# Kernel optimization log

Hardware: AMD Instinct MI355X
Metric: run time of the kernel (lower is better)

Reference implementation:

```python
import jax, jax.numpy as jnp
import numpy as np

N = 100000   # nodes
E = 1600000  # edges
IN = 128     # in_node_channels
H = 128      # hidden_channels
EPS = 1e-5   # BatchNorm eps


def _gcn_conv(x, W, b, src, dst, n):
    # x' = W x, then symmetric-normalized aggregation with self-loops (PyG GCNConv)
    xw = x @ W                                             # [N, H]
    loop = jnp.arange(n, dtype=src.dtype)
    src_f = jnp.concatenate([src, loop])                   # [E+N]
    dst_f = jnp.concatenate([dst, loop])
    deg = jax.ops.segment_sum(jnp.ones(src_f.shape, xw.dtype), dst_f, num_segments=n)
    dis = jax.lax.rsqrt(jnp.maximum(deg, 1.0))             # deg >= 1 due to self-loops
    norm = dis[src_f] * dis[dst_f]                         # [E+N]
    msg = xw[src_f] * norm[:, None]                        # gather + scale
    out = jax.ops.segment_sum(msg, dst_f, num_segments=n)  # scatter-add
    return out + b


def _bn(x, gamma, beta):
    # training-mode BatchNorm1d over the node dimension
    m = jnp.mean(x, axis=0)
    v = jnp.mean(jnp.square(x - m), axis=0)
    return gamma * (x - m) * jax.lax.rsqrt(v + EPS) + beta


def setup_inputs() -> dict:
    key = jax.random.key(0)
    ks = jax.random.split(key, 8)
    glorot = lambda k, shape, fan: jax.random.normal(k, shape, jnp.float32) / np.sqrt(fan).astype(np.float32)
    x = jax.random.normal(ks[0], (N, IN), jnp.float32)
    edge_index = jax.random.randint(ks[1], (2, E), 0, N, dtype=jnp.int32)
    return {
        "x": x,
        "edge_index": edge_index,
        "W1": glorot(ks[2], (IN, H), IN), "b1": jnp.zeros((H,), jnp.float32),
        "g1": jnp.ones((H,), jnp.float32), "be1": jnp.zeros((H,), jnp.float32),
        "W2": glorot(ks[3], (H, H), H), "b2": jnp.zeros((H,), jnp.float32),
        "g2": jnp.ones((H,), jnp.float32), "be2": jnp.zeros((H,), jnp.float32),
        "Wm1": glorot(ks[4], (H, 64), H), "bm1": jnp.zeros((64,), jnp.float32),
        "Wm2": glorot(ks[5], (64, 1), 64), "bm2": jnp.zeros((1,), jnp.float32),
    }


def reference(x, edge_index, W1, b1, g1, be1, W2, b2, g2, be2, Wm1, bm1, Wm2, bm2):
    src, dst = edge_index[0], edge_index[1]
    h = jax.nn.relu(_bn(_gcn_conv(x, W1, b1, src, dst, N), g1, be1))
    h = jax.nn.relu(_bn(_gcn_conv(h, W2, b2, src, dst, N), g2, be2))
    # MLP head (dropout is identity in eval / deterministic reference)
    h = jax.nn.relu(h @ Wm1 + bm1)
    out = h @ Wm2 + bm2                                     # [N, 1]
    return jnp.squeeze(out, axis=-1)                        # [N]
```

## Files before the change

kernel.cpp:

```cpp
#include <hip/hip_runtime.h>
#include <hip/hip_fp16.h>

#define HC 128
#define EPS_BN 1e-5f
#define NSTRIPE 8
#define AGG_BLOCKS 3072
#define BSHIFT 9
#define BNODES (1 << BSHIFT)
#define BCAP 12288
#define CHUNK 8192
#define SRC_BITS 18

typedef _Float16 f16;
typedef f16  f16x8 __attribute__((ext_vector_type(8)));
typedef float f32x4 __attribute__((ext_vector_type(4)));

__global__ void prologue(const float* __restrict__ W1, const float* __restrict__ W2,
                         const float* __restrict__ Wm1,
                         f16* __restrict__ Wt1, f16* __restrict__ Wt2,
                         f16* __restrict__ Wm1t, f16* __restrict__ padrow,
                         int* __restrict__ gcur, float* __restrict__ stats) {
    int idx = blockIdx.x * 256 + threadIdx.x;
    if (idx < 16384) {
        int k = idx >> 7, c = idx & 127;
        Wt1[(size_t)c * HC + k] = (f16)W1[idx];
    } else if (idx < 32768) {
        int i = idx - 16384;
        int k = i >> 7, c = i & 127;
        Wt2[(size_t)c * HC + k] = (f16)W2[i];
    } else if (idx < 40960) {
        int i = idx - 32768;
        int c = i >> 7, k = i & 127;
        Wm1t[(size_t)c * HC + k] = (f16)Wm1[(size_t)k * 64 + c];
    } else if (idx < 41088) {
        padrow[idx - 40960] = (f16)0.f;
    } else if (idx < 41344) {
        int b = idx - 41088;
        gcur[b] = b * BCAP;
    } else if (idx < 45440) {
        stats[idx - 41344] = 0.f;
    }
}

__global__ __launch_bounds__(1024) void edge_bin(const int* __restrict__ src,
                                                 const int* __restrict__ dst,
                                                 int* __restrict__ gcur,
                                                 unsigned int* __restrict__ packed, int E) {
    __shared__ int cnt[256];
    __shared__ int cur[256];
    const int tid = threadIdx.x;
    const int e0 = blockIdx.x * CHUNK;
    if (tid < 256) cnt[tid] = 0;
    __syncthreads();
    for (int i = tid; i < CHUNK; i += 1024) {
        int e = e0 + i;
        if (e < E) atomicAdd(&cnt[dst[e] >> BSHIFT], 1);
    }
    __syncthreads();
    if (tid < 256) cur[tid] = (cnt[tid] > 0) ? atomicAdd(&gcur[tid], cnt[tid]) : 0;
    __syncthreads();
    for (int i = tid; i < CHUNK; i += 1024) {
        int e = e0 + i;
        if (e < E) {
            int s = src[e], d = dst[e];
            int pos = atomicAdd(&cur[d >> BSHIFT], 1);
            packed[pos] = ((unsigned)(d & (BNODES - 1)) << SRC_BITS) | (unsigned)s;
        }
    }
}

__global__ __launch_bounds__(1024) void edge_sort(const unsigned int* __restrict__ packed,
                                                  const int* __restrict__ gcur,
                                                  int2* __restrict__ rowptr2,
                                                  float* __restrict__ dis,
                                                  int* __restrict__ srcs, int n) {
    __shared__ int cnt[BNODES];
    __shared__ int cur[BNODES];
    __shared__ int scn[BNODES];
    const int b = blockIdx.x;
    const int node0 = b << BSHIFT;
    const int tid = threadIdx.x;
    const int base = b * BCAP;
    const int end  = gcur[b];

    if (tid < BNODES) cnt[tid] = 0;
    __syncthreads();
    for (int e = base + tid; e < end; e += 1024)
        atomicAdd(&cnt[packed[e] >> SRC_BITS], 1);
    __syncthreads();
    if (tid < BNODES) scn[tid] = cnt[tid];
    __syncthreads();
    for (int off = 1; off < BNODES; off <<= 1) {
        int t = 0;
        if (tid < BNODES && tid >= off) t = scn[tid - off];
        __syncthreads();
        if (tid < BNODES) scn[tid] += t;
        __syncthreads();
    }
    if (tid < BNODES) {
        int excl = scn[tid] - cnt[tid];
        int node = node0 + tid;
        if (node < n) {
            rowptr2[node] = make_int2(base + excl, base + excl + cnt[tid]);
            dis[node] = rsqrtf((float)cnt[tid] + 1.f);
        }
        cur[tid] = excl;
    }
    __syncthreads();
    for (int e = base + tid; e < end; e += 1024) {
        unsigned p = packed[e];
        int pos = atomicAdd(&cur[p >> SRC_BITS], 1);
        srcs[base + pos] = (int)(p & ((1u << SRC_BITS) - 1));
    }
}

template<int SRC_F16, int TRANS>
__global__ __launch_bounds__(256) void gemm_mfma(const void* __restrict__ Xv,
                                                 const f16* __restrict__ Wt,
                                                 const float* __restrict__ stats,
                                                 const float* __restrict__ gamma,
                                                 const float* __restrict__ beta,
                                                 const float* __restrict__ dis,
                                                 f16* __restrict__ Y, int n) {
    __shared__ f16 Ah[64][136];
    __shared__ f16 Bh[128][136];
    __shared__ float sc[HC], sh[HC];
    const int tid  = threadIdx.x;
    const int row0 = blockIdx.x * 64;

    if constexpr (TRANS) {
        if (tid < 128) {
            float s = 0.f, q = 0.f;
#pragma unroll
            for (int t = 0; t < NSTRIPE; ++t) {
                s += stats[t * 256 + tid];
                q += stats[t * 256 + 128 + tid];
            }
            float m = s / (float)n;
            float v = q / (float)n - m * m;
            float scv = gamma[tid] * rsqrtf(fmaxf(v, 0.f) + EPS_BN);
            sc[tid] = scv;
            sh[tid] = beta[tid] - m * scv;
        }
    }

#pragma unroll
    for (int i = 0; i < 8; ++i) {
        int idx = i * 256 + tid;
        int r = idx >> 4, g = idx & 15;
        *(f16x8*)&Bh[r][g * 8] = *(const f16x8*)(Wt + (size_t)r * HC + g * 8);
    }
    __syncthreads();

#pragma unroll
    for (int i = 0; i < 4; ++i) {
        int idx = i * 256 + tid;
        int r = idx >> 4, g = idx & 15;
        int grow = row0 + r;
        f16x8 h = {};
        if (grow < n) {
            if constexpr (SRC_F16) {
                f16x8 v = *(const f16x8*)((const f16*)Xv + (size_t)grow * HC + g * 8);
                if constexpr (TRANS) {
#pragma unroll
                    for (int j = 0; j < 8; ++j) {
                        float f = (float)v[j];
                        f = fmaxf(fmaf(f, sc[g * 8 + j], sh[g * 8 + j]), 0.f);
                        h[j] = (f16)f;
                    }
                } else h = v;
            } else {
                const float* X = (const float*)Xv;
                float4 a = *(const float4*)(X + (size_t)grow * HC + g * 8);
                float4 c = *(const float4*)(X + (size_t)grow * HC + g * 8 + 4);
                h[0] = (f16)a.x; h[1] = (f16)a.y; h[2] = (f16)a.z; h[3] = (f16)a.w;
                h[4] = (f16)c.x; h[5] = (f16)c.y; h[6] = (f16)c.z; h[7] = (f16)c.w;
            }
        }
        *(f16x8*)&Ah[r][g * 8] = h;
    }
    __syncthreads();

    const int wv   = tid >> 6;
    const int lane = tid & 63;
    const int m    = lane & 15;
    const int kq   = (lane >> 4) * 8;

    f32x4 acc[8] = {};
#pragma unroll
    for (int kc = 0; kc < HC; kc += 32) {
        f16x8 a = *(const f16x8*)&Ah[wv * 16 + m][kc + kq];
#pragma unroll
        for (int t = 0; t < 8; ++t) {
            f16x8 b = *(const f16x8*)&Bh[t * 16 + m][kc + kq];
            acc[t] = __builtin_amdgcn_mfma_f32_16x16x32_f16(a, b, acc[t], 0, 0, 0);
        }
    }

    const int rbase = row0 + wv * 16 + (lane >> 4) * 4;
#pragma unroll
    for (int r = 0; r < 4; ++r) {
        int grow = rbase + r;
        if (grow < n) {
            float dv = dis[grow];
#pragma unroll
            for (int t = 0; t < 8; ++t)
                Y[(size_t)grow * HC + t * 16 + m] = (f16)(acc[t][r] * dv);
        }
    }
}

__global__ __launch_bounds__(256) void gcn_agg_f16(const f16* __restrict__ xws,
                                                   const int* __restrict__ srcs,
                                                   const int2* __restrict__ rowptr2,
                                                   const float* __restrict__ dis,
                                                   const float* __restrict__ bias,
                                                   f16* __restrict__ out,
                                                   float* __restrict__ stats,
                                                   int n, int nwaves) {
    __shared__ float lds_s[4][128], lds_q[4][128];
    const int wv   = threadIdx.x >> 6;
    const int lane = threadIdx.x & 63;
    const int g    = lane >> 4;
    const int cg   = lane & 15;

    float b8[8];
#pragma unroll
    for (int j = 0; j < 8; ++j) b8[j] = bias[cg * 8 + j];

    float s8[8] = {}, q8[8] = {};

    for (int node = blockIdx.x * 4 + wv; node < n; node += nwaves) {
        const int2 rp = rowptr2[node];
        const int e1 = rp.y;
        float acc[8] = {};
        for (int e = rp.x; e < e1; e += 8) {
            int i0 = e + g, i1 = e + g + 4;
            int s0 = (i0 < e1) ? srcs[i0] : n;
            int s1 = (i1 < e1) ? srcs[i1] : n;
            f16x8 v0 = *(const f16x8*)(xws + (size_t)s0 * HC + cg * 8);
            f16x8 v1 = *(const f16x8*)(xws + (size_t)s1 * HC + cg * 8);
#pragma unroll
            for (int j = 0; j < 8; ++j) {
                acc[j] += (float)v0[j];
                acc[j] += (float)v1[j];
            }
        }
#pragma unroll
        for (int j = 0; j < 8; ++j) acc[j] += __shfl_xor(acc[j], 16);
#pragma unroll
        for (int j = 0; j < 8; ++j) acc[j] += __shfl_xor(acc[j], 32);

        if (g == 0) {
            float dv = dis[node];
            f16x8 self = *(const f16x8*)(xws + (size_t)node * HC + cg * 8);
            f16x8 o;
#pragma unroll
            for (int j = 0; j < 8; ++j) {
                float r = fmaf(acc[j] + (float)self[j], dv, b8[j]);
                o[j] = (f16)r;
                s8[j] += r;
                q8[j] += r * r;
            }
            *(f16x8*)(out + (size_t)node * HC + cg * 8) = o;
        }
    }

    if (g == 0) {
#pragma unroll
        for (int j = 0; j < 8; ++j) {
            lds_s[wv][cg * 8 + j] = s8[j];
            lds_q[wv][cg * 8 + j] = q8[j];
        }
    }
    __syncthreads();
    float* stripe = stats + (size_t)(blockIdx.x & (NSTRIPE - 1)) * 256;
    if (threadIdx.x < 128) {
        float s = lds_s[0][threadIdx.x] + lds_s[1][threadIdx.x] +
                  lds_s[2][threadIdx.x] + lds_s[3][threadIdx.x];
        float q = lds_q[0][threadIdx.x] + lds_q[1][threadIdx.x] +
                  lds_q[2][threadIdx.x] + lds_q[3][threadIdx.x];
        atomicAdd(&stripe[threadIdx.x], s);
        atomicAdd(&stripe[128 + threadIdx.x], q);
    }
}

__global__ __launch_bounds__(256) void mlp_mfma(const f16* __restrict__ h,
                                                const float* __restrict__ stats,
                                                const float* __restrict__ gamma,
                                                const float* __restrict__ beta,
                                                const f16* __restrict__ Wm1t,
                                                const float* __restrict__ bm1,
                                                const float* __restrict__ Wm2,
                                                const float* __restrict__ bm2,
                                                float* __restrict__ out, int n) {
    __shared__ f16 Hs[64][136];
    __shared__ f16 Ws[64][136];
    __shared__ float sc[HC], sh[HC], bmv[64], w2v[64];
    const int tid  = threadIdx.x;
    const int row0 = blockIdx.x * 64;

    if (tid < 128) {
        float s = 0.f, q = 0.f;
#pragma unroll
        for (int t = 0; t < NSTRIPE; ++t) {
            s += stats[t * 256 + tid];
            q += stats[t * 256 + 128 + tid];
        }
        float m = s / (float)n;
        float v = q / (float)n - m * m;
        float scv = gamma[tid] * rsqrtf(fmaxf(v, 0.f) + EPS_BN);
        sc[tid] = scv;
        sh[tid] = beta[tid] - m * scv;
    }
    if (tid < 64) { bmv[tid] = bm1[tid]; w2v[tid] = Wm2[tid]; }

#pragma unroll
    for (int i = 0; i < 4; ++i) {
        int idx = i * 256 + tid;
        int r = idx >> 4, g = idx & 15;
        *(f16x8*)&Ws[r][g * 8] = *(const f16x8*)(Wm1t + (size_t)r * HC + g * 8);
    }
    __syncthreads();

#pragma unroll
    for (int i = 0; i < 4; ++i) {
        int idx = i * 256 + tid;
        int r = idx >> 4, g = idx & 15;
        int grow = row0 + r;
        f16x8 hv = {};
        if (grow < n) {
            f16x8 v = *(const f16x8*)(h + (size_t)grow * HC + g * 8);
#pragma unroll
            for (int j = 0; j < 8; ++j) {
                float f = (float)v[j];
                f = fmaxf(fmaf(f, sc[g * 8 + j], sh[g * 8 + j]), 0.f);
                hv[j] = (f16)f;
            }
        }
        *(f16x8*)&Hs[r][g * 8] = hv;
    }
    __syncthreads();

    const int wv   = tid >> 6;
    const int lane = tid & 63;
    const int m    = lane & 15;
    const int kq   = (lane >> 4) * 8;

    f32x4 acc[4] = {};
#pragma unroll
    for (int kc = 0; kc < HC; kc += 32) {
        f16x8 a = *(const f16x8*)&Hs[wv * 16 + m][kc + kq];
#pragma unroll
        for (int t = 0; t < 4; ++t) {
            f16x8 b = *(const f16x8*)&Ws[t * 16 + m][kc + kq];
            acc[t] = __builtin_amdgcn_mfma_f32_16x16x32_f16(a, b, acc[t], 0, 0, 0);
        }
    }

    float part[4];
#pragma unroll
    for (int reg = 0; reg < 4; ++reg) {
        float s = 0.f;
#pragma unroll
        for (int t = 0; t < 4; ++t) {
            int col = t * 16 + m;
            s += fmaxf(acc[t][reg] + bmv[col], 0.f) * w2v[col];
        }
        part[reg] = s;
    }
#pragma unroll
    for (int off = 1; off < 16; off <<= 1) {
#pragma unroll
        for (int reg = 0; reg < 4; ++reg)
            part[reg] += __shfl_xor(part[reg], off);
    }
    if (m == 0) {
        int rbase = row0 + wv * 16 + (lane >> 4) * 4;
        float bb = bm2[0];
#pragma unroll
        for (int reg = 0; reg < 4; ++reg) {
            int row = rbase + reg;
            if (row < n) out[row] = part[reg] + bb;
        }
    }
}

extern "C" void kernel_launch(void* const* d_in, const int* in_sizes, int n_in,
                              void* d_out, int out_size, void* d_ws, size_t ws_size,
                              hipStream_t stream) {
    const float* x   = (const float*)d_in[0];
    const int*   ei  = (const int*)  d_in[1];
    const float* W1  = (const float*)d_in[2];
    const float* b1  = (const float*)d_in[3];
    const float* g1  = (const float*)d_in[4];
    const float* be1 = (const float*)d_in[5];
    const float* W2  = (const float*)d_in[6];
    const float* b2  = (const float*)d_in[7];
    const float* g2  = (const float*)d_in[8];
    const float* be2 = (const float*)d_in[9];
    const float* Wm1 = (const float*)d_in[10];
    const float* bm1 = (const float*)d_in[11];
    const float* Wm2 = (const float*)d_in[12];
    const float* bm2 = (const float*)d_in[13];
    float* out = (float*)d_out;

    const int n = in_sizes[0] / HC;
    const int E = in_sizes[1] / 2;
    const int* srcp = ei;
    const int* dstp = ei + E;
    const int nb = (n + BNODES - 1) >> BSHIFT;

    char* ws = (char*)d_ws;
    size_t off = 0;
    auto alloc = [&](size_t bytes) { void* p = ws + off; off = (off + bytes + 511) & ~511ULL; return p; };
    float*  dis     = (float*) alloc((size_t)n * 4);
    int2*   rowptr2 = (int2*)  alloc((size_t)n * 8);
    int*    gcur    = (int*)   alloc(1024);
    float*  stats   = (float*) alloc(2 * NSTRIPE * 256 * 4);
    float*  stats1  = stats;
    float*  stats2  = stats + NSTRIPE * 256;
    unsigned int* packed = (unsigned int*)alloc((size_t)nb * BCAP * 4);
    int*    srcs    = (int*)   alloc((size_t)nb * BCAP * 4);
    f16*    xws     = (f16*)   alloc((size_t)(n + 1) * HC * 2);
    f16*    bufBh   = (f16*)   alloc((size_t)n * HC * 2);
    f16*    Wt1     = (f16*)   alloc((size_t)HC * HC * 2);
    f16*    Wt2     = (f16*)   alloc((size_t)HC * HC * 2);
    f16*    Wm1t    = (f16*)   alloc((size_t)64 * HC * 2);

    const int gemmBlocks = (n + 63) / 64;
    const int binBlocks  = (E + CHUNK - 1) / CHUNK;
    const int aggWaves   = AGG_BLOCKS * 4;

    prologue<<<(45440 + 255) / 256, 256, 0, stream>>>(W1, W2, Wm1, Wt1, Wt2, Wm1t,
                                                      xws + (size_t)n * HC, gcur, stats);

    edge_bin<<<binBlocks, 1024, 0, stream>>>(srcp, dstp, gcur, packed, E);
    edge_sort<<<nb, 1024, 0, stream>>>(packed, gcur, rowptr2, dis, srcs, n);

    gemm_mfma<0, 0><<<gemmBlocks, 256, 0, stream>>>(x, Wt1, nullptr, nullptr, nullptr,
                                                    dis, xws, n);
    gcn_agg_f16<<<AGG_BLOCKS, 256, 0, stream>>>(xws, srcs, rowptr2, dis, b1,
                                                bufBh, stats1, n, aggWaves);

    gemm_mfma<1, 1><<<gemmBlocks, 256, 0, stream>>>(bufBh, Wt2, stats1, g1, be1,
                                                    dis, xws, n);
    gcn_agg_f16<<<AGG_BLOCKS, 256, 0, stream>>>(xws, srcs, rowptr2, dis, b2,
                                                bufBh, stats2, n, aggWaves);

    mlp_mfma<<<gemmBlocks, 256, 0, stream>>>(bufBh, stats2, g2, be2, Wm1t, bm1, Wm2, bm2,
                                             out, n);
}
```

Measured before the change: 318.7 us.

## Move weight prep into sort kernel, cache dst in registers, stage GEMM stores via LDS

Shrinks the prologue to a single-block init and folds the weight transpose/convert into extra blocks of the edge sort kernel, so that work shares a launch with the sort. edge_bin keeps the dst values in registers between its two passes instead of reading them again from global memory. The GEMM epilogue writes its scaled results to LDS and then stores full 16-byte rows, replacing scattered 2-byte stores. The LDS staging adds extra barriers, and the Ah tile must be large enough to hold the output layout.

```diff
diff --git a/kernel.cpp b/kernel.cpp
--- a/kernel.cpp
+++ b/kernel.cpp
@@ -15,31 +15,13 @@
 typedef f16  f16x8 __attribute__((ext_vector_type(8)));
 typedef float f32x4 __attribute__((ext_vector_type(4)));
 
-__global__ void prologue(const float* __restrict__ W1, const float* __restrict__ W2,
-                         const float* __restrict__ Wm1,
-                         f16* __restrict__ Wt1, f16* __restrict__ Wt2,
-                         f16* __restrict__ Wm1t, f16* __restrict__ padrow,
-                         int* __restrict__ gcur, float* __restrict__ stats) {
-    int idx = blockIdx.x * 256 + threadIdx.x;
-    if (idx < 16384) {
-        int k = idx >> 7, c = idx & 127;
-        Wt1[(size_t)c * HC + k] = (f16)W1[idx];
-    } else if (idx < 32768) {
-        int i = idx - 16384;
-        int k = i >> 7, c = i & 127;
-        Wt2[(size_t)c * HC + k] = (f16)W2[i];
-    } else if (idx < 40960) {
-        int i = idx - 32768;
-        int c = i >> 7, k = i & 127;
-        Wm1t[(size_t)c * HC + k] = (f16)Wm1[(size_t)k * 64 + c];
-    } else if (idx < 41088) {
-        padrow[idx - 40960] = (f16)0.f;
-    } else if (idx < 41344) {
-        int b = idx - 41088;
-        gcur[b] = b * BCAP;
-    } else if (idx < 45440) {
-        stats[idx - 41344] = 0.f;
-    }
+__global__ __launch_bounds__(1024) void init_small(int* __restrict__ gcur,
+                                                   float* __restrict__ stats,
+                                                   f16* __restrict__ padrow) {
+    int tid = threadIdx.x;
+    if (tid < 256) gcur[tid] = tid * BCAP;
+    if (tid < 128) padrow[tid] = (f16)0.f;
+    for (int i = tid; i < 2 * NSTRIPE * 256; i += 1024) stats[i] = 0.f;
 }
 
 __global__ __launch_bounds__(1024) void edge_bin(const int* __restrict__ src,
@@ -50,30 +32,56 @@
     __shared__ int cur[256];
     const int tid = threadIdx.x;
     const int e0 = blockIdx.x * CHUNK;
+    int dreg[8];
     if (tid < 256) cnt[tid] = 0;
     __syncthreads();
-    for (int i = tid; i < CHUNK; i += 1024) {
-        int e = e0 + i;
-        if (e < E) atomicAdd(&cnt[dst[e] >> BSHIFT], 1);
+#pragma unroll
+    for (int i = 0; i < 8; ++i) {
+        int e = e0 + i * 1024 + tid;
+        dreg[i] = (e < E) ? dst[e] : -1;
+        if (dreg[i] >= 0) atomicAdd(&cnt[dreg[i] >> BSHIFT], 1);
     }
     __syncthreads();
     if (tid < 256) cur[tid] = (cnt[tid] > 0) ? atomicAdd(&gcur[tid], cnt[tid]) : 0;
     __syncthreads();
-    for (int i = tid; i < CHUNK; i += 1024) {
-        int e = e0 + i;
-        if (e < E) {
-            int s = src[e], d = dst[e];
-            int pos = atomicAdd(&cur[d >> BSHIFT], 1);
-            packed[pos] = ((unsigned)(d & (BNODES - 1)) << SRC_BITS) | (unsigned)s;
-        }
-    }
-}
-
-__global__ __launch_bounds__(1024) void edge_sort(const unsigned int* __restrict__ packed,
-                                                  const int* __restrict__ gcur,
-                                                  int2* __restrict__ rowptr2,
-                                                  float* __restrict__ dis,
-                                                  int* __restrict__ srcs, int n) {
+#pragma unroll
+    for (int i = 0; i < 8; ++i) {
+        int e = e0 + i * 1024 + tid;
+        if (dreg[i] >= 0) {
+            int s = src[e];
+            int pos = atomicAdd(&cur[dreg[i] >> BSHIFT], 1);
+            packed[pos] = ((unsigned)(dreg[i] & (BNODES - 1)) << SRC_BITS) | (unsigned)s;
+        }
+    }
+}
+
+__global__ __launch_bounds__(1024) void sort_wprep(const unsigned int* __restrict__ packed,
+                                                   const int* __restrict__ gcur,
+                                                   int2* __restrict__ rowptr2,
+                                                   float* __restrict__ dis,
+                                                   int* __restrict__ srcs, int n, int nbSort,
+                                                   const float* __restrict__ W1,
+                                                   const float* __restrict__ W2,
+                                                   const float* __restrict__ Wm1,
+                                                   f16* __restrict__ Wt1,
+                                                   f16* __restrict__ Wt2,
+                                                   f16* __restrict__ Wm1t) {
+    if (blockIdx.x >= nbSort) {
+        int idx = (blockIdx.x - nbSort) * 1024 + threadIdx.x;
+        if (idx < 16384) {
+            int k = idx >> 7, c = idx & 127;
+            Wt1[(size_t)c * HC + k] = (f16)W1[idx];
+        } else if (idx < 32768) {
+            int i = idx - 16384;
+            int k = i >> 7, c = i & 127;
+            Wt2[(size_t)c * HC + k] = (f16)W2[i];
+        } else if (idx < 40960) {
+            int i = idx - 32768;
+            int c = i >> 7, k = i & 127;
+            Wm1t[(size_t)c * HC + k] = (f16)Wm1[(size_t)k * 64 + c];
+        }
+        return;
+    }
     __shared__ int cnt[BNODES];
     __shared__ int cur[BNODES];
     __shared__ int scn[BNODES];
@@ -197,16 +205,29 @@
         }
     }
 
-    const int rbase = row0 + wv * 16 + (lane >> 4) * 4;
-#pragma unroll
-    for (int r = 0; r < 4; ++r) {
-        int grow = rbase + r;
-        if (grow < n) {
-            float dv = dis[grow];
-#pragma unroll
-            for (int t = 0; t < 8; ++t)
-                Y[(size_t)grow * HC + t * 16 + m] = (f16)(acc[t][r] * dv);
-        }
+    __syncthreads();
+    {
+        const int rg = (lane >> 4) * 4;
+        float dv[4];
+#pragma unroll
+        for (int r = 0; r < 4; ++r) {
+            int grow = row0 + wv * 16 + rg + r;
+            dv[r] = (grow < n) ? dis[grow] : 0.f;
+        }
+#pragma unroll
+        for (int t = 0; t < 8; ++t)
+#pragma unroll
+            for (int r = 0; r < 4; ++r)
+                Ah[wv * 16 + rg + r][t * 16 + m] = (f16)(acc[t][r] * dv[r]);
+    }
+    __syncthreads();
+#pragma unroll
+    for (int i = 0; i < 4; ++i) {
+        int idx = i * 256 + tid;
+        int r = idx >> 4, g = idx & 15;
+        int grow = row0 + r;
+        if (grow < n)
+            *(f16x8*)(Y + (size_t)grow * HC + g * 8) = *(const f16x8*)&Ah[r][g * 8];
     }
 }
 
@@ -430,13 +451,14 @@
 
     const int gemmBlocks = (n + 63) / 64;
     const int binBlocks  = (E + CHUNK - 1) / CHUNK;
+    const int wprepBlks  = 40;
     const int aggWaves   = AGG_BLOCKS * 4;
 
-    prologue<<<(45440 + 255) / 256, 256, 0, stream>>>(W1, W2, Wm1, Wt1, Wt2, Wm1t,
-                                                      xws + (size_t)n * HC, gcur, stats);
+    init_small<<<1, 1024, 0, stream>>>(gcur, stats, xws + (size_t)n * HC);
 
     edge_bin<<<binBlocks, 1024, 0, stream>>>(srcp, dstp, gcur, packed, E);
-    edge_sort<<<nb, 1024, 0, stream>>>(packed, gcur, rowptr2, dis, srcs, n);
+    sort_wprep<<<nb + wprepBlks, 1024, 0, stream>>>(packed, gcur, rowptr2, dis, srcs, n, nb,
+                                                    W1, W2, Wm1, Wt1, Wt2, Wm1t);
 
     gemm_mfma<0, 0><<<gemmBlocks, 256, 0, stream>>>(x, Wt1, nullptr, nullptr, nullptr,
                                                     dis, xws, n);
```

Measured after the change: 315.1 us. About the same (-1.2%).
